# Optimization experiments

Measured on AMD Instinct MI355X. Metric: run time of the kernel, lower is better.

Reference implementation:

```python
import jax, jax.numpy as jnp
import numpy as np

N_NODES = 100000
N_ADJ = 11
E = 1600000
D_IN = 128
D_OUT = 16
C = 1.0
MIN_NORM = 1e-15
PROJ_EPS = 4e-3  # float32 eps used by HGCN PoincareBall.proj


def _norm(x):
    return jnp.maximum(jnp.linalg.norm(x, axis=-1, keepdims=True), MIN_NORM)


def _artanh(x):
    return jnp.arctanh(jnp.clip(x, -1.0 + 1e-7, 1.0 - 1e-7))


def logmap0(x, c):
    sqrt_c = c ** 0.5
    xn = _norm(x)
    return x / xn / sqrt_c * _artanh(sqrt_c * xn)


def expmap0(u, c):
    sqrt_c = c ** 0.5
    un = _norm(u)
    return jnp.tanh(sqrt_c * un) * u / (sqrt_c * un)


def proj(x, c):
    xn = _norm(x)
    maxnorm = (1.0 - PROJ_EPS) / (c ** 0.5)
    return jnp.where(xn > maxnorm, x / xn * maxnorm, x)


def setup_inputs() -> dict:
    key = jax.random.key(0)
    k1, k2, k3, k4, k5, k6 = jax.random.split(key, 6)
    # points inside the Poincare ball (||x|| << 1)
    x = jax.random.normal(k1, (N_NODES, D_IN), dtype=jnp.float32) * 0.01
    adj_rows = jax.random.randint(k2, (N_ADJ, E), 0, N_NODES, dtype=jnp.int32)
    adj_cols = jax.random.randint(k3, (N_ADJ, E), 0, N_NODES, dtype=jnp.int32)
    adj_vals = jax.random.uniform(k4, (N_ADJ, E), dtype=jnp.float32) * (1.0 / 16.0)
    fan_in = D_IN
    bound = float(np.sqrt(6.0 / fan_in))  # kaiming_uniform-ish scale
    adj_weight = jax.random.uniform(k5, (N_ADJ, D_IN, D_OUT), dtype=jnp.float32,
                                    minval=-bound, maxval=bound)
    bias = jax.random.normal(k6, (D_OUT,), dtype=jnp.float32) * 0.01
    return {"x": x, "adj_rows": adj_rows, "adj_cols": adj_cols,
            "adj_vals": adj_vals, "adj_weight": adj_weight, "bias": bias}


def reference(x, adj_rows, adj_cols, adj_vals, adj_weight, bias):
    n = x.shape[0]
    x_tangent = logmap0(x, C)                      # [N, D_IN]
    acc = jnp.zeros((n, D_OUT), dtype=x.dtype)
    for i in range(N_ADJ):                          # fixed small relation loop
        support_t = x_tangent @ adj_weight[i]       # [N, 16]
        gathered = support_t[adj_cols[i]] * adj_vals[i][:, None]  # [E, 16]
        agg = jax.ops.segment_sum(gathered, adj_rows[i], num_segments=n)
        acc = acc + proj(expmap0(agg, C), C)
    return acc / 11.0 + bias
```

## Files before the change

kernel.cpp:

```cpp
#include <hip/hip_runtime.h>
#include <hip/hip_fp16.h>
#include <math.h>

#define NN 100000
#define NADJ 11
#define EE 1600000
#define DI 128
#define DO 16

#define NBINS 391
#define BCAP 8
#define SEGCAP 4608

static constexpr float MIN_NORM = 1e-15f;
static constexpr float MAXNORM  = 1.0f - 4e-3f;

typedef float nf2 __attribute__((ext_vector_type(2)));
typedef float nf4 __attribute__((ext_vector_type(4)));

__global__ void k_scale(const float* __restrict__ x, float* __restrict__ scale) {
    int lane   = threadIdx.x & 63;
    int wid    = (blockIdx.x * blockDim.x + threadIdx.x) >> 6;
    int nwav   = (gridDim.x * blockDim.x) >> 6;
    for (int n = wid; n < NN; n += nwav) {
        float2 v = ((const float2*)(x + (size_t)n * DI))[lane];
        float ss = v.x * v.x + v.y * v.y;
        #pragma unroll
        for (int off = 1; off < 64; off <<= 1) ss += __shfl_xor(ss, off);
        if (lane == 0) {
            float xn = fmaxf(sqrtf(ss), MIN_NORM);
            float xc = fminf(xn, 1.0f - 1e-7f);
            scale[n] = atanhf(xc) / xn;
        }
    }
}

template<int G>
__global__ __launch_bounds__(256, 2) void k_gemm(const float* __restrict__ x,
                                                 const float* __restrict__ scale,
                                                 const float* __restrict__ W,
                                                 __half* __restrict__ support) {
    constexpr int COLS = 16 * G;
    __shared__ float xs[64][36];
    __shared__ float ws[COLS][36];
    const int t  = threadIdx.x;
    const int tc = t & 15;
    const int tr = t >> 4;
    const int n0 = blockIdx.x * 64;

    float acc[4][G];
    #pragma unroll
    for (int m = 0; m < 4; ++m)
        #pragma unroll
        for (int j = 0; j < G; ++j) acc[m][j] = 0.f;

    for (int kb = 0; kb < 4; ++kb) {
        __syncthreads();
        for (int idx = t; idx < 64 * 8; idx += 256) {
            int r = idx >> 3, k4 = idx & 7;
            int n = n0 + r;
            float4 v = make_float4(0.f, 0.f, 0.f, 0.f);
            if (n < NN) v = ((const float4*)(x + (size_t)n * DI + kb * 32))[k4];
            *(float4*)&xs[r][k4 * 4] = v;
        }
        for (int idx = t; idx < G * 32 * 4; idx += 256) {
            int j = idx >> 7, rem = idx & 127, kk = rem >> 2, o4 = rem & 3;
            float4 v = *(const float4*)(W + ((size_t)j * DI + kb * 32 + kk) * DO + o4 * 4);
            ws[j * 16 + o4 * 4 + 0][kk] = v.x;
            ws[j * 16 + o4 * 4 + 1][kk] = v.y;
            ws[j * 16 + o4 * 4 + 2][kk] = v.z;
            ws[j * 16 + o4 * 4 + 3][kk] = v.w;
        }
        __syncthreads();
        #pragma unroll
        for (int kk4 = 0; kk4 < 8; ++kk4) {
            float4 xv[4];
            #pragma unroll
            for (int m = 0; m < 4; ++m) xv[m] = *(const float4*)&xs[tr * 4 + m][kk4 * 4];
            #pragma unroll
            for (int j = 0; j < G; ++j) {
                float4 wv = *(const float4*)&ws[j * 16 + tc][kk4 * 4];
                #pragma unroll
                for (int m = 0; m < 4; ++m)
                    acc[m][j] += xv[m].x * wv.x + xv[m].y * wv.y
                               + xv[m].z * wv.z + xv[m].w * wv.w;
            }
        }
    }
    float sv[4];
    #pragma unroll
    for (int m = 0; m < 4; ++m) {
        int n = n0 + tr * 4 + m;
        sv[m] = (n < NN) ? scale[n] : 0.f;
    }
    float* st = &xs[0][0];
    const int row = t >> 2, q = t & 3;
    for (int j = 0; j < G; ++j) {
        __syncthreads();
        #pragma unroll
        for (int m = 0; m < 4; ++m)
            st[(tr * 4 + m) * 17 + tc] = acc[m][j] * sv[m];
        __syncthreads();
        int n = n0 + row;
        if (n < NN) {
            __half2 h0 = __floats2half2_rn(st[row * 17 + q * 4 + 0],
                                           st[row * 17 + q * 4 + 1]);
            __half2 h1 = __floats2half2_rn(st[row * 17 + q * 4 + 2],
                                           st[row * 17 + q * 4 + 3]);
            uint2 u;
            u.x = *(unsigned*)&h0;
            u.y = *(unsigned*)&h1;
            *(uint2*)&support[((size_t)j * NN + n) * DO + q * 4] = u;
        }
    }
}

__global__ __launch_bounds__(256) void k_bin(const int* __restrict__ rows,
                                             const int* __restrict__ cols,
                                             const float* __restrict__ vals,
                                             int* __restrict__ gcur,
                                             float2* __restrict__ packed) {
    __shared__ int    cnt[NBINS];
    __shared__ float2 buf[NBINS][BCAP];
    __shared__ int    fl_b[256];
    __shared__ int    fl_gp[256];
    __shared__ int    nflush;

    const int t  = threadIdx.x;
    const int ro = blockIdx.y;
    const size_t ebase = (size_t)ro * EE;
    int*    cur = gcur + (size_t)ro * NBINS;
    float2* pk  = packed + (size_t)ro * NBINS * SEGCAP;

    const int nper = (EE + gridDim.x - 1) / gridDim.x;
    const int e0 = blockIdx.x * nper;
    const int e1 = (e0 + nper < EE) ? e0 + nper : EE;

    for (int b = t; b < NBINS; b += 256) cnt[b] = 0;
    __syncthreads();

    for (int eb = e0; eb < e1; eb += 256) {
        int e = eb + t;
        if (e < e1) {
            int   r = __builtin_nontemporal_load(&rows[ebase + e]);
            int   c = __builtin_nontemporal_load(&cols[ebase + e]);
            float v = __builtin_nontemporal_load(&vals[ebase + e]);
            int bin = r >> 8;
            float ptag = __uint_as_float(((unsigned)(r & 255) << 17) | (unsigned)c);
            int pos = atomicAdd(&cnt[bin], 1);
            if (pos < BCAP) {
                buf[bin][pos] = make_float2(v, ptag);
            } else {
                int gp = atomicAdd(&cur[bin], 1);
                if (gp < SEGCAP) pk[(size_t)bin * SEGCAP + gp] = make_float2(v, ptag);
            }
        }
        __syncthreads();
        if (t == 0) nflush = 0;
        __syncthreads();
        for (int b = t; b < NBINS; b += 256) {
            int c = cnt[b];
            if (c >= BCAP) {
                int i = atomicAdd(&nflush, 1);
                fl_b[i]  = b;
                fl_gp[i] = atomicAdd(&cur[b], BCAP);
                cnt[b] = 0;
            }
        }
        __syncthreads();
        int nf = nflush, o = t & 7;
        for (int j = t >> 3; j < nf; j += 32) {
            int b = fl_b[j];
            int gp = fl_gp[j] + o;
            if (gp < SEGCAP) pk[(size_t)b * SEGCAP + gp] = buf[b][o];
        }
        __syncthreads();
    }
    int o = t & 7;
    for (int b = t >> 3; b < NBINS; b += 32) {
        int c = cnt[b];
        int gp0 = 0;
        if (o == 0 && c > 0) gp0 = atomicAdd(&cur[b], c);
        gp0 = __shfl(gp0, (threadIdx.x & 63) & ~7);
        if (o < c) {
            int gp = gp0 + o;
            if (gp < SEGCAP) pk[(size_t)b * SEGCAP + gp] = buf[b][o];
        }
    }
}

__global__ __launch_bounds__(256) void k_agg(const int* __restrict__ gcur,
                                             const float2* __restrict__ packed,
                                             const __half* __restrict__ support,
                                             float* __restrict__ agg, int r0) {
    __shared__ float acc[128 * 17];
    const int bx   = blockIdx.x;
    const int bin  = bx % NBINS;
    const int hr   = bx / NBINS;
    const int half = hr & 1;
    const int ro   = hr >> 1;
    const int t = threadIdx.x;
    const int o = t & 15;
    const int g = t >> 4;

    for (int i = t; i < 128 * 17; i += 256) acc[i] = 0.f;
    __syncthreads();

    int c = gcur[(size_t)ro * NBINS + bin];
    if (c > SEGCAP) c = SEGCAP;
    const float2* seg = packed + ((size_t)ro * NBINS + bin) * SEGCAP;
    const __half* sup = support + (size_t)(r0 + ro) * NN * DO;

    const int nb = c >> 3;
    for (int b = g; b < nb; b += 16) {
        const nf4* s4 = (const nf4*)&seg[b * 8];
        nf4 s0 = __builtin_nontemporal_load(&s4[0]);
        nf4 s1 = __builtin_nontemporal_load(&s4[1]);
        nf4 s2 = __builtin_nontemporal_load(&s4[2]);
        nf4 s3 = __builtin_nontemporal_load(&s4[3]);
        float    v[8];
        unsigned p[8];
        v[0] = s0.x; p[0] = __float_as_uint(s0.y);
        v[1] = s0.z; p[1] = __float_as_uint(s0.w);
        v[2] = s1.x; p[2] = __float_as_uint(s1.y);
        v[3] = s1.z; p[3] = __float_as_uint(s1.w);
        v[4] = s2.x; p[4] = __float_as_uint(s2.y);
        v[5] = s2.z; p[5] = __float_as_uint(s2.w);
        v[6] = s3.x; p[6] = __float_as_uint(s3.y);
        v[7] = s3.z; p[7] = __float_as_uint(s3.w);
        float sv[8];
        bool  keep[8];
        #pragma unroll
        for (int k = 0; k < 8; ++k) {
            keep[k] = (int)(p[k] >> 24) == half;
            sv[k] = keep[k] ? __half2float(sup[(size_t)(p[k] & 0x1FFFFu) * DO + o]) : 0.f;
        }
        #pragma unroll
        for (int k = 0; k < 8; ++k)
            if (keep[k])
                atomicAdd(&acc[((p[k] >> 17) & 127u) * 17 + o], v[k] * sv[k]);
    }
    if (g == 0) {
        for (int i = nb * 8; i < c; ++i) {
            float2 e = seg[i];
            unsigned p = __float_as_uint(e.y);
            if ((int)(p >> 24) == half)
                atomicAdd(&acc[((p >> 17) & 127u) * 17 + o],
                          e.x * __half2float(sup[(size_t)(p & 0x1FFFFu) * DO + o]));
        }
    }
    __syncthreads();

    const int n0 = bin * 256 + half * 128;
    const int row0 = t >> 2, q = t & 3;
    #pragma unroll
    for (int pass = 0; pass < 2; ++pass) {
        int r = pass * 64 + row0;
        int n = n0 + r;
        if (n < NN) {
            nf4 v;
            v.x = acc[r * 17 + q * 4 + 0];
            v.y = acc[r * 17 + q * 4 + 1];
            v.z = acc[r * 17 + q * 4 + 2];
            v.w = acc[r * 17 + q * 4 + 3];
            __builtin_nontemporal_store(v, (nf4*)&agg[((size_t)ro * NN + n) * DO + q * 4]);
        }
    }
}

__global__ __launch_bounds__(256) void k_final(const float* __restrict__ agg,
                                               float* __restrict__ out, int nrel) {
    int t = blockIdx.x * blockDim.x + threadIdx.x;
    int n = t >> 4, o = t & 15;
    if (n >= NN) return;
    float oa = 0.f;
    for (int ro = 0; ro < nrel; ++ro) {
        float u = __builtin_nontemporal_load(&agg[((size_t)ro * NN + n) * DO + o]);
        float ss = u * u;
        ss += __shfl_xor(ss, 1, 16);
        ss += __shfl_xor(ss, 2, 16);
        ss += __shfl_xor(ss, 4, 16);
        ss += __shfl_xor(ss, 8, 16);
        float un = fmaxf(sqrtf(ss), MIN_NORM);
        float th = tanhf(un);
        float rn = fmaxf(th, MIN_NORM);
        float sc = (rn > MAXNORM) ? (MAXNORM / rn) : 1.0f;
        oa += u * (th / un) * sc;
    }
    out[(size_t)n * DO + o] += oa * (1.0f / 11.0f);
}

__global__ void k_init_out(const float* __restrict__ bias, float* __restrict__ out) {
    int idx = blockIdx.x * blockDim.x + threadIdx.x;
    if (idx < NN * 16) out[idx] = bias[idx & 15];
}

extern "C" void kernel_launch(void* const* d_in, const int* in_sizes, int n_in,
                              void* d_out, int out_size, void* d_ws, size_t ws_size,
                              hipStream_t stream) {
    const float* x        = (const float*)d_in[0];
    const int*   adj_rows = (const int*)d_in[1];
    const int*   adj_cols = (const int*)d_in[2];
    const float* adj_vals = (const float*)d_in[3];
    const float* adj_w    = (const float*)d_in[4];
    const float* bias     = (const float*)d_in[5];
    float*       out      = (float*)d_out;

    char* p = (char*)d_ws;
    auto alloc = [&](size_t bytes) {
        char* r = p;
        p += (bytes + 255) & ~(size_t)255;
        return r;
    };
    float*  scale   = (float*)alloc((size_t)NN * 4);
    __half* support = (__half*)alloc((size_t)NADJ * NN * DO * 2);

    size_t used    = (size_t)(p - (char*)d_ws);
    size_t per_rel = ((size_t)NBINS * 4 + 256)
                   + ((size_t)NBINS * SEGCAP * 8 + 256)
                   + ((size_t)NN * DO * 4 + 256);
    size_t avail   = (ws_size > used) ? ws_size - used : 0;
    int cr = (int)(avail / per_rel);
    if (cr < 1) cr = 1;
    if (cr > NADJ) cr = NADJ;
    int*    gcur   = (int*)alloc((size_t)cr * NBINS * 4);
    float2* packed = (float2*)alloc((size_t)cr * NBINS * SEGCAP * 8);
    float*  agg    = (float*)alloc((size_t)cr * NN * DO * 4);

    k_scale<<<512, 256, 0, stream>>>(x, scale);
    k_init_out<<<(NN * 16 + 255) / 256, 256, 0, stream>>>(bias, out);
    k_gemm<6><<<(NN + 63) / 64, 256, 0, stream>>>(x, scale, adj_w, support);
    k_gemm<5><<<(NN + 63) / 64, 256, 0, stream>>>(x, scale,
                                                  adj_w + (size_t)6 * DI * DO,
                                                  support + (size_t)6 * NN * DO);

    for (int r0 = 0; r0 < NADJ; r0 += cr) {
        int nr = (NADJ - r0 < cr) ? (NADJ - r0) : cr;
        hipMemsetAsync(gcur, 0, (size_t)nr * NBINS * 4, stream);
        k_bin<<<dim3(192, nr), 256, 0, stream>>>(adj_rows + (size_t)r0 * EE,
                                                 adj_cols + (size_t)r0 * EE,
                                                 adj_vals + (size_t)r0 * EE,
                                                 gcur, packed);
        k_agg<<<NBINS * 2 * nr, 256, 0, stream>>>(gcur, packed, support, agg, r0);
        k_final<<<(NN * 16 + 255) / 256, 256, 0, stream>>>(agg, out, nr);
    }
}
```

Before: 2.103 ms.

## Split k_agg bins into quarters and launch per relation

Each aggregation block now covers a quarter of a 256-node bin (64 rows) instead of a half, which halves the shared accumulator and doubles the number of blocks per relation. The edge segment is therefore scanned four times instead of twice, with each block filtering on two bits of the packed word. Aggregation is now launched once per relation rather than as one grid, segment loads are cached rather than nontemporal, and k_gemm's launch bound occupancy hint goes from 2 to 3. The intent is more parallelism and lighter LDS use, paid for by redundant segment reads and extra launches.

```diff
diff --git a/kernel.cpp b/kernel.cpp
--- a/kernel.cpp
+++ b/kernel.cpp
@@ -36,7 +36,7 @@
 }
 
 template<int G>
-__global__ __launch_bounds__(256, 2) void k_gemm(const float* __restrict__ x,
+__global__ __launch_bounds__(256, 3) void k_gemm(const float* __restrict__ x,
                                                  const float* __restrict__ scale,
                                                  const float* __restrict__ W,
                                                  __half* __restrict__ support) {
@@ -192,18 +192,17 @@
 __global__ __launch_bounds__(256) void k_agg(const int* __restrict__ gcur,
                                              const float2* __restrict__ packed,
                                              const __half* __restrict__ support,
-                                             float* __restrict__ agg, int r0) {
-    __shared__ float acc[128 * 17];
-    const int bx   = blockIdx.x;
-    const int bin  = bx % NBINS;
-    const int hr   = bx / NBINS;
-    const int half = hr & 1;
-    const int ro   = hr >> 1;
+                                             float* __restrict__ agg,
+                                             int r0, int ro) {
+    __shared__ float acc[64 * 17];
+    const int bx      = blockIdx.x;
+    const int bin     = bx >> 2;
+    const int quarter = bx & 3;
     const int t = threadIdx.x;
     const int o = t & 15;
     const int g = t >> 4;
 
-    for (int i = t; i < 128 * 17; i += 256) acc[i] = 0.f;
+    for (int i = t; i < 64 * 17; i += 256) acc[i] = 0.f;
     __syncthreads();
 
     int c = gcur[(size_t)ro * NBINS + bin];
@@ -213,11 +212,8 @@
 
     const int nb = c >> 3;
     for (int b = g; b < nb; b += 16) {
-        const nf4* s4 = (const nf4*)&seg[b * 8];
-        nf4 s0 = __builtin_nontemporal_load(&s4[0]);
-        nf4 s1 = __builtin_nontemporal_load(&s4[1]);
-        nf4 s2 = __builtin_nontemporal_load(&s4[2]);
-        nf4 s3 = __builtin_nontemporal_load(&s4[3]);
+        const float4* s4 = (const float4*)&seg[b * 8];
+        float4 s0 = s4[0], s1 = s4[1], s2 = s4[2], s3 = s4[3];
         float    v[8];
         unsigned p[8];
         v[0] = s0.x; p[0] = __float_as_uint(s0.y);
@@ -232,39 +228,35 @@
         bool  keep[8];
         #pragma unroll
         for (int k = 0; k < 8; ++k) {
-            keep[k] = (int)(p[k] >> 24) == half;
+            keep[k] = (int)((p[k] >> 23) & 3u) == quarter;
             sv[k] = keep[k] ? __half2float(sup[(size_t)(p[k] & 0x1FFFFu) * DO + o]) : 0.f;
         }
         #pragma unroll
         for (int k = 0; k < 8; ++k)
             if (keep[k])
-                atomicAdd(&acc[((p[k] >> 17) & 127u) * 17 + o], v[k] * sv[k]);
+                atomicAdd(&acc[((p[k] >> 17) & 63u) * 17 + o], v[k] * sv[k]);
     }
     if (g == 0) {
         for (int i = nb * 8; i < c; ++i) {
             float2 e = seg[i];
             unsigned p = __float_as_uint(e.y);
-            if ((int)(p >> 24) == half)
-                atomicAdd(&acc[((p >> 17) & 127u) * 17 + o],
+            if ((int)((p >> 23) & 3u) == quarter)
+                atomicAdd(&acc[((p >> 17) & 63u) * 17 + o],
                           e.x * __half2float(sup[(size_t)(p & 0x1FFFFu) * DO + o]));
         }
     }
     __syncthreads();
 
-    const int n0 = bin * 256 + half * 128;
-    const int row0 = t >> 2, q = t & 3;
-    #pragma unroll
-    for (int pass = 0; pass < 2; ++pass) {
-        int r = pass * 64 + row0;
-        int n = n0 + r;
-        if (n < NN) {
-            nf4 v;
-            v.x = acc[r * 17 + q * 4 + 0];
-            v.y = acc[r * 17 + q * 4 + 1];
-            v.z = acc[r * 17 + q * 4 + 2];
-            v.w = acc[r * 17 + q * 4 + 3];
-            __builtin_nontemporal_store(v, (nf4*)&agg[((size_t)ro * NN + n) * DO + q * 4]);
-        }
+    const int n0 = bin * 256 + quarter * 64;
+    const int row = t >> 2, q = t & 3;
+    int n = n0 + row;
+    if (n < NN) {
+        nf4 v;
+        v.x = acc[row * 17 + q * 4 + 0];
+        v.y = acc[row * 17 + q * 4 + 1];
+        v.z = acc[row * 17 + q * 4 + 2];
+        v.w = acc[row * 17 + q * 4 + 3];
+        __builtin_nontemporal_store(v, (nf4*)&agg[((size_t)ro * NN + n) * DO + q * 4]);
     }
 }
 
@@ -341,7 +333,8 @@
                                                  adj_cols + (size_t)r0 * EE,
                                                  adj_vals + (size_t)r0 * EE,
                                                  gcur, packed);
-        k_agg<<<NBINS * 2 * nr, 256, 0, stream>>>(gcur, packed, support, agg, r0);
+        for (int ro = 0; ro < nr; ++ro)
+            k_agg<<<NBINS * 4, 256, 0, stream>>>(gcur, packed, support, agg, r0, ro);
         k_final<<<(NN * 16 + 255) / 256, 256, 0, stream>>>(agg, out, nr);
     }
 }
```

New measurement: 2.814 ms. +33.8%, slower.
